# Performance work log

Measured on AMD Instinct MI355X. Metric: run time of the kernel, lower is better.

Reference implementation:

```python
import jax, jax.numpy as jnp
import numpy as np

S = 7          # grid cells per side (CFG['CELL_NUMS'])
L_COORD = 5.0  # CFG['L_COORD']
L_NOOBJ = 0.5  # CFG['L_NOOBJ']
N_BATCH = 16384


def setup_inputs() -> dict:
    key = jax.random.key(0)
    k1, k2, k3 = jax.random.split(key, 3)
    pred = jax.random.uniform(k1, (N_BATCH, S, S, 30), dtype=jnp.float32)
    target = jax.random.uniform(k2, (N_BATCH, S, S, 30), dtype=jnp.float32)
    obj = jax.random.uniform(k3, (N_BATCH, S, S)) < 0.3
    target = target.at[..., 4].set(jnp.where(obj, target[..., 4], 0.0))
    target = target.at[..., 9].set(jnp.where(obj, target[..., 9], 0.0))
    return {"pred_tensor": pred, "target_tensor": target}


def _yolo_v1_loss(pred, target):
    # pred/target: [N, S, S, 30] = [2 boxes x (x,y,w,h,c), 20 class probs]
    N = pred.shape[0]
    coo_f = (target[..., 4] > 0).astype(pred.dtype)   # [N,S,S] object cells
    noo_f = 1.0 - coo_f                                # no-object cells

    # no-object loss: confidence channels 4 and 9 on noo cells (sum-MSE)
    nooobj_loss = jnp.sum(
        noo_f * ((pred[..., 4] - target[..., 4]) ** 2
                 + (pred[..., 9] - target[..., 9]) ** 2))

    # class loss over object cells (sum-MSE over 20 classes)
    class_loss = jnp.sum(coo_f[..., None] * (pred[..., 10:] - target[..., 10:]) ** 2)

    # boxes: [N,S,S,2,5]
    pb = pred[..., :10].reshape(N, S, S, 2, 5)
    tb = target[..., :10].reshape(N, S, S, 2, 5)

    # xywh -> xyxy for the 2 predicted boxes and the first target box per cell
    p_lt = pb[..., :2] - 0.5 * pb[..., 2:4]
    p_rb = pb[..., :2] + 0.5 * pb[..., 2:4]
    t0 = tb[..., 0, :]                                 # target box used for IOU
    t_lt = t0[..., :2] - 0.5 * t0[..., 2:4]
    t_rb = t0[..., :2] + 0.5 * t0[..., 2:4]

    # NOTE: faithful reproduction of the source's compute_iou, including its
    # bug: wh = (rb - lt < 0).float(), so 'inter' is an indicator product.
    lt = jnp.maximum(p_lt, t_lt[..., None, :])         # [N,S,S,2,2]
    rb = jnp.minimum(p_rb, t_rb[..., None, :])
    wh_ind = (rb - lt < 0).astype(pred.dtype)
    inter = wh_ind[..., 0] * wh_ind[..., 1]            # [N,S,S,2]
    area1 = (p_rb[..., 0] - p_lt[..., 0]) * (p_rb[..., 1] - p_lt[..., 1])
    area2 = ((t_rb[..., 0] - t_lt[..., 0]) * (t_rb[..., 1] - t_lt[..., 1]))[..., None]
    iou = inter / (area1 + area2 - inter)              # [N,S,S,2]

    # responsible box = argmax IOU over the 2 predicted boxes per cell
    idx = jnp.argmax(iou, axis=-1)                     # [N,S,S]
    gather = idx[..., None, None]                      # [N,S,S,1,1]
    resp_p = jnp.take_along_axis(pb, gather, axis=3)[..., 0, :]  # [N,S,S,5]
    resp_t = jnp.take_along_axis(tb, gather, axis=3)[..., 0, :]

    contain_loss = jnp.sum(coo_f * (resp_p[..., 4] - resp_t[..., 4]) ** 2)

    # guard sqrt at masked-out cells so 0*d(sqrt(0)) does not produce NaN grads
    safe = coo_f[..., None] > 0
    sqrt_wp = jnp.sqrt(jnp.where(safe, resp_p[..., 2:4], 1.0))
    sqrt_wt = jnp.sqrt(jnp.where(safe, resp_t[..., 2:4], 1.0))
    loc_loss = (jnp.sum(coo_f[..., None] * (resp_p[..., :2] - resp_t[..., :2]) ** 2)
                + jnp.sum(coo_f[..., None] * (sqrt_wp - sqrt_wt) ** 2))

    return (L_COORD * loc_loss + contain_loss + L_NOOBJ * nooobj_loss + class_loss) / N


def reference(pred_tensor, target_tensor):
    return _yolo_v1_loss(pred_tensor, target_tensor)
```

## Files before the change

### kernel.cpp

```cpp
#include <hip/hip_runtime.h>


#define CH 30
#define CPB 256
#define T 256
#define TILE_F (CPB * CH)
#define TILE_V4 (TILE_F / 4)

typedef __attribute__((address_space(3))) void* lds_vp;
typedef const __attribute__((address_space(1))) void* gvp;

__global__ __launch_bounds__(T, 4)
void yolo_partial(const float* __restrict__ pred,
                  const float* __restrict__ targ,
                  float* __restrict__ partial) {
    __shared__ float tile[TILE_F];
    __shared__ float wave_sums[T / 64];

    const int tid = threadIdx.x;
    const long long fbase = (long long)blockIdx.x * TILE_F;

    {
        const float4* gt = (const float4*)(targ + fbase);
#pragma unroll
        for (int k = 0; k < 8; ++k) {
            const int v = tid + k * T;
            if (v < TILE_V4)
                __builtin_amdgcn_global_load_lds((gvp)(gt + v), (lds_vp)(tile + v * 4),
                                                 16, 0, 0);
        }
    }
    __syncthreads();

    float2 t01, t23, t45, t67, t89, tc[10];
    {
        const float2* t2 = (const float2*)(tile + tid * CH);
        t01 = t2[0]; t23 = t2[1]; t45 = t2[2]; t67 = t2[3]; t89 = t2[4];
#pragma unroll
        for (int k = 0; k < 10; ++k) tc[k] = t2[5 + k];
    }
    __syncthreads();

    {
        const float4* gp = (const float4*)(pred + fbase);
#pragma unroll
        for (int k = 0; k < 8; ++k) {
            const int v = tid + k * T;
            if (v < TILE_V4)
                __builtin_amdgcn_global_load_lds((gvp)(gp + v), (lds_vp)(tile + v * 4),
                                                 16, 0, 0);
        }
    }
    __syncthreads();

    float sum = 0.0f;
    {
        const float2* p2 = (const float2*)(tile + tid * CH);
        const float2 p01 = p2[0], p23 = p2[1], p45 = p2[2], p67 = p2[3], p89 = p2[4];

        const float t4 = t45.x, t9 = t89.y;
        const bool coo = t4 > 0.0f;

        const float d4 = p45.x - t4;
        const float d9 = p89.y - t9;
        sum = coo ? 0.0f : 0.5f * (d4 * d4 + d9 * d9);

        if (coo) {
            float cl = 0.0f;
#pragma unroll
            for (int k = 0; k < 10; ++k) {
                const float2 pc = p2[5 + k];
                const float dx = pc.x - tc[k].x;
                const float dy = pc.y - tc[k].y;
                cl += dx * dx + dy * dy;
            }
            sum += cl;

            const float tltx = t01.x - 0.5f * t23.x;
            const float tlty = t01.y - 0.5f * t23.y;
            const float trbx = t01.x + 0.5f * t23.x;
            const float trby = t01.y + 0.5f * t23.y;
            const float area2 = (trbx - tltx) * (trby - tlty);

            const float b0x = p01.x, b0y = p01.y, b0w = p23.x, b0h = p23.y;
            const float b1x = p45.y, b1y = p67.x, b1w = p67.y, b1h = p89.x;

            float iou0, iou1;
            {
                const float pltx = b0x - 0.5f * b0w, plty = b0y - 0.5f * b0h;
                const float prbx = b0x + 0.5f * b0w, prby = b0y + 0.5f * b0h;
                const float ltx = fmaxf(pltx, tltx), lty = fmaxf(plty, tlty);
                const float rbx = fminf(prbx, trbx), rby = fminf(prby, trby);
                const float inter = ((rbx - ltx < 0.0f) ? 1.0f : 0.0f) *
                                    ((rby - lty < 0.0f) ? 1.0f : 0.0f);
                const float area1 = (prbx - pltx) * (prby - plty);
                iou0 = inter / (area1 + area2 - inter);
            }
            {
                const float pltx = b1x - 0.5f * b1w, plty = b1y - 0.5f * b1h;
                const float prbx = b1x + 0.5f * b1w, prby = b1y + 0.5f * b1h;
                const float ltx = fmaxf(pltx, tltx), lty = fmaxf(plty, tlty);
                const float rbx = fminf(prbx, trbx), rby = fminf(prby, trby);
                const float inter = ((rbx - ltx < 0.0f) ? 1.0f : 0.0f) *
                                    ((rby - lty < 0.0f) ? 1.0f : 0.0f);
                const float area1 = (prbx - pltx) * (prby - plty);
                iou1 = inter / (area1 + area2 - inter);
            }
            const bool idx1 = iou1 > iou0;

            const float rpx = idx1 ? b1x : b0x;
            const float rpy = idx1 ? b1y : b0y;
            const float rpw = idx1 ? b1w : b0w;
            const float rph = idx1 ? b1h : b0h;
            const float rpc = idx1 ? p89.y : p45.x;
            const float rtx = idx1 ? t45.y : t01.x;
            const float rty = idx1 ? t67.x : t01.y;
            const float rtw = idx1 ? t67.y : t23.x;
            const float rth = idx1 ? t89.x : t23.y;
            const float rtc = idx1 ? t89.y : t45.x;

            const float dc = rpc - rtc;
            sum += dc * dc;

            const float dx = rpx - rtx;
            const float dy = rpy - rty;
            const float dw = sqrtf(rpw) - sqrtf(rtw);
            const float dh = sqrtf(rph) - sqrtf(rth);
            sum += 5.0f * (dx * dx + dy * dy + dw * dw + dh * dh);
        }
    }

#pragma unroll
    for (int off = 32; off > 0; off >>= 1)
        sum += __shfl_down(sum, off, 64);
    const int wave = tid >> 6;
    const int lane = tid & 63;
    if (lane == 0) wave_sums[wave] = sum;
    __syncthreads();
    if (tid == 0) {
        float tot = 0.0f;
#pragma unroll
        for (int w = 0; w < T / 64; ++w) tot += wave_sums[w];
        partial[blockIdx.x] = tot;
    }
}

__global__ __launch_bounds__(256)
void yolo_reduce(const float* __restrict__ partial, int n, float* __restrict__ out) {
    __shared__ float wave_sums[4];
    float s = 0.0f;
    const int n4 = n >> 2;
    const float4* p4 = (const float4*)partial;
    for (int v = threadIdx.x; v < n4; v += 256) {
        const float4 x = p4[v];
        s += (x.x + x.y) + (x.z + x.w);
    }
    for (int v = (n4 << 2) + threadIdx.x; v < n; v += 256)
        s += partial[v];
#pragma unroll
    for (int off = 32; off > 0; off >>= 1)
        s += __shfl_down(s, off, 64);
    const int wave = threadIdx.x >> 6;
    const int lane = threadIdx.x & 63;
    if (lane == 0) wave_sums[wave] = s;
    __syncthreads();
    if (threadIdx.x == 0) {
        const float tot = wave_sums[0] + wave_sums[1] + wave_sums[2] + wave_sums[3];
        out[0] = tot * (1.0f / 16384.0f);
    }
}

extern "C" void kernel_launch(void* const* d_in, const int* in_sizes, int n_in,
                              void* d_out, int out_size, void* d_ws, size_t ws_size,
                              hipStream_t stream) {
    const float* pred = (const float*)d_in[0];
    const float* targ = (const float*)d_in[1];
    float* out = (float*)d_out;
    float* partial = (float*)d_ws;

    const int n_cells = in_sizes[0] / CH;
    const int blocks = n_cells / CPB;

    yolo_partial<<<blocks, T, 0, stream>>>(pred, targ, partial);
    yolo_reduce<<<1, 256, 0, stream>>>(partial, blocks, out);
}
```

Baseline: 204.2 us.

## Give each wave a private LDS region and drop block-wide barriers

Each wave now loads its own 32 cells of both target and prediction into a private LDS region, waits only on its own vmcnt, and computes with half its lanes. This removes the two-phase load with three block-wide __syncthreads and lets the target and prediction loads be in flight together. The trade-off is that half the lanes sit idle during compute, blocks cover half as many cells (so twice as many blocks), and launch bounds are raised to 5.

```diff
diff --git a/kernel.cpp b/kernel.cpp
--- a/kernel.cpp
+++ b/kernel.cpp
@@ -2,60 +2,56 @@
 
 
 #define CH 30
-#define CPB 256
+#define CPW 32
+#define WAVES 4
 #define T 256
-#define TILE_F (CPB * CH)
-#define TILE_V4 (TILE_F / 4)
+#define CPB (CPW * WAVES)
+#define WREG_F (CPW * CH * 2)
+#define INPUT_F (CPW * CH)
 
 typedef __attribute__((address_space(3))) void* lds_vp;
 typedef const __attribute__((address_space(1))) void* gvp;
 
-__global__ __launch_bounds__(T, 4)
+__global__ __launch_bounds__(T, 5)
 void yolo_partial(const float* __restrict__ pred,
                   const float* __restrict__ targ,
                   float* __restrict__ partial) {
-    __shared__ float tile[TILE_F];
-    __shared__ float wave_sums[T / 64];
+    __shared__ float tile[WAVES * WREG_F];
+    __shared__ float wave_sums[WAVES];
 
     const int tid = threadIdx.x;
-    const long long fbase = (long long)blockIdx.x * TILE_F;
+    const int wave = tid >> 6;
+    const int lane = tid & 63;
 
-    {
-        const float4* gt = (const float4*)(targ + fbase);
+    float* wreg = &tile[wave * WREG_F];
+    const long long cell0 = (long long)blockIdx.x * CPB + wave * CPW;
+    const float* gt = targ + cell0 * CH;
+    const float* gp = pred + cell0 * CH;
+
 #pragma unroll
-        for (int k = 0; k < 8; ++k) {
-            const int v = tid + k * T;
-            if (v < TILE_V4)
-                __builtin_amdgcn_global_load_lds((gvp)(gt + v), (lds_vp)(tile + v * 4),
-                                                 16, 0, 0);
-        }
+    for (int k = 0; k < 3; ++k) {
+        const int idx = k * 64 + lane;
+        __builtin_amdgcn_global_load_lds((gvp)(gt + idx * 4),
+                                         (lds_vp)(wreg + idx * 4), 16, 0, 0);
+        __builtin_amdgcn_global_load_lds((gvp)(gp + idx * 4),
+                                         (lds_vp)(wreg + INPUT_F + idx * 4), 16, 0, 0);
     }
-    __syncthreads();
+    if (lane < 48) {
+        const int idx = 192 + lane;
+        __builtin_amdgcn_global_load_lds((gvp)(gt + idx * 4),
+                                         (lds_vp)(wreg + idx * 4), 16, 0, 0);
+        __builtin_amdgcn_global_load_lds((gvp)(gp + idx * 4),
+                                         (lds_vp)(wreg + INPUT_F + idx * 4), 16, 0, 0);
+    }
 
-    float2 t01, t23, t45, t67, t89, tc[10];
-    {
-        const float2* t2 = (const float2*)(tile + tid * CH);
-        t01 = t2[0]; t23 = t2[1]; t45 = t2[2]; t67 = t2[3]; t89 = t2[4];
-#pragma unroll
-        for (int k = 0; k < 10; ++k) tc[k] = t2[5 + k];
-    }
-    __syncthreads();
-
-    {
-        const float4* gp = (const float4*)(pred + fbase);
-#pragma unroll
-        for (int k = 0; k < 8; ++k) {
-            const int v = tid + k * T;
-            if (v < TILE_V4)
-                __builtin_amdgcn_global_load_lds((gvp)(gp + v), (lds_vp)(tile + v * 4),
-                                                 16, 0, 0);
-        }
-    }
-    __syncthreads();
+    asm volatile("s_waitcnt vmcnt(0)" ::: "memory");
 
     float sum = 0.0f;
-    {
-        const float2* p2 = (const float2*)(tile + tid * CH);
+    if (lane < CPW) {
+        const float2* t2 = (const float2*)(wreg + lane * CH);
+        const float2* p2 = (const float2*)(wreg + INPUT_F + lane * CH);
+
+        const float2 t01 = t2[0], t23 = t2[1], t45 = t2[2], t67 = t2[3], t89 = t2[4];
         const float2 p01 = p2[0], p23 = p2[1], p45 = p2[2], p67 = p2[3], p89 = p2[4];
 
         const float t4 = t45.x, t9 = t89.y;
@@ -70,8 +66,9 @@
 #pragma unroll
             for (int k = 0; k < 10; ++k) {
                 const float2 pc = p2[5 + k];
-                const float dx = pc.x - tc[k].x;
-                const float dy = pc.y - tc[k].y;
+                const float2 tc = t2[5 + k];
+                const float dx = pc.x - tc.x;
+                const float dy = pc.y - tc.y;
                 cl += dx * dx + dy * dy;
             }
             sum += cl;
@@ -133,14 +130,12 @@
 #pragma unroll
     for (int off = 32; off > 0; off >>= 1)
         sum += __shfl_down(sum, off, 64);
-    const int wave = tid >> 6;
-    const int lane = tid & 63;
     if (lane == 0) wave_sums[wave] = sum;
     __syncthreads();
     if (tid == 0) {
         float tot = 0.0f;
 #pragma unroll
-        for (int w = 0; w < T / 64; ++w) tot += wave_sums[w];
+        for (int w = 0; w < WAVES; ++w) tot += wave_sums[w];
         partial[blockIdx.x] = tot;
     }
 }
```

Result: no change. 204.7 us (+0.3%).
